# Kernel tuning notes

Measured on AMD Instinct MI355X. Metric: run time of the kernel, lower is better.

## Reference

```python
import jax, jax.numpy as jnp
import numpy as np

B, LQ, LK = 4, 2048, 2048
XS, YS, PD = 1024, 1024, 128


def setup_inputs() -> dict:
    key = jax.random.key(0)
    ks = jax.random.split(key, 8)
    s_x = 1.0 / np.sqrt(XS)
    s_y = 1.0 / np.sqrt(YS)
    return {
        "x": jax.random.normal(ks[0], (B, LQ, XS), dtype=jnp.float32),
        "y": jax.random.normal(ks[1], (B, LK, YS), dtype=jnp.float32),
        "Wq": jax.random.normal(ks[2], (XS, PD), dtype=jnp.float32) * s_x,
        "bq": jax.random.normal(ks[3], (PD,), dtype=jnp.float32) * 0.01,
        "Wk": jax.random.normal(ks[4], (YS, PD), dtype=jnp.float32) * s_y,
        "bk": jax.random.normal(ks[5], (PD,), dtype=jnp.float32) * 0.01,
        "Wv": jax.random.normal(ks[6], (YS, PD), dtype=jnp.float32) * s_y,
        "bv": jax.random.normal(ks[7], (PD,), dtype=jnp.float32) * 0.01,
        "mask": 1,
    }


def reference(x, y, Wq, bq, Wk, bk, Wv, bv, mask):
    # Projections (torch Linear: x @ W^T + b; here weights stored as [in, out])
    q = x @ Wq + bq  # [B, LQ, PD]
    k = y @ Wk + bk  # [B, LK, PD]
    v = y @ Wv + bv  # [B, LK, PD]
    scale = 1.0 / jnp.sqrt(jnp.asarray(PD, dtype=q.dtype))
    att = jax.nn.softmax(jnp.einsum("bqd,bkd->bqk", q, k) * scale, axis=-1)
    if mask:
        # NOTE: faithful to original — triu applied AFTER softmax (diagonal=1),
        # zeroing the lower triangle + diagonal without renormalizing.
        att = jnp.triu(att, k=1)
    return jnp.einsum("bqk,bkd->bqd", att, v)  # [B, LQ, PD]
```

## Files before the change

### kernel.cpp

```cpp
#include <hip/hip_runtime.h>

typedef short s8v __attribute__((ext_vector_type(8)));
typedef float f4v __attribute__((ext_vector_type(4)));

#define NB 4
#define LQ 2048
#define LKK 2048
#define XS 1024
#define PDD 128

#define PST 68
#define AST 132

__device__ __forceinline__ ushort f2bf(float x) {
  union { float f; uint u; } v; v.f = x;
  uint r = (v.u + 0x7fffu + ((v.u >> 16) & 1u)) >> 16;
  return (ushort)r;
}

__global__ __launch_bounds__(256) void k_wtrans(const float* __restrict__ Wq,
                                                const float* __restrict__ Wk,
                                                const float* __restrict__ Wv,
                                                ushort* __restrict__ Wt) {
  int p = blockIdx.y;
  const float* W = (p == 0) ? Wq : (p == 1) ? Wk : Wv;
  ushort* out = Wt + (size_t)p * (PDD * XS);
  int t = threadIdx.x;
  int n = t >> 1;
  int kk0 = (t & 1) * 16;
  int k0 = blockIdx.x * 32;
  ushort tmp[16];
#pragma unroll
  for (int i = 0; i < 16; ++i) tmp[i] = f2bf(W[(size_t)(k0 + kk0 + i) * PDD + n]);
  uint4 u0, u1;
  u0.x = tmp[0] | ((uint)tmp[1] << 16);  u0.y = tmp[2] | ((uint)tmp[3] << 16);
  u0.z = tmp[4] | ((uint)tmp[5] << 16);  u0.w = tmp[6] | ((uint)tmp[7] << 16);
  u1.x = tmp[8] | ((uint)tmp[9] << 16);  u1.y = tmp[10] | ((uint)tmp[11] << 16);
  u1.z = tmp[12] | ((uint)tmp[13] << 16); u1.w = tmp[14] | ((uint)tmp[15] << 16);
  uint4* dst = (uint4*)&out[n * XS + k0 + kk0];
  dst[0] = u0; dst[1] = u1;
}

__global__ __launch_bounds__(256, 3) void k_proj(const float* __restrict__ x,
                                                 const float* __restrict__ y,
                                                 const ushort* __restrict__ Wt,
                                                 const float* __restrict__ bq,
                                                 const float* __restrict__ bk,
                                                 const float* __restrict__ bv,
                                                 ushort* __restrict__ qo,
                                                 ushort* __restrict__ ko,
                                                 ushort* __restrict__ vt) {
  int bx = blockIdx.x;
  int p = bx >> 8;
  int tile = bx & 255;
  const float* in = (p == 0) ? x : y;
  const ushort* wt = Wt + (size_t)p * (PDD * XS);
  int row0 = tile * 32;
  __shared__ ushort As[32 * 72];
  __shared__ ushort Bs[128 * 72];
  int t = threadIdx.x, wave = t >> 6, lane = t & 63, quad = lane >> 4, lc = lane & 15;

  int ar = t >> 3, ac0 = (t & 7) * 8;
  int bn = t >> 1, bk0 = (t & 1) * 32;
  const float* asrc = in + (size_t)(row0 + ar) * XS + ac0;
  const ushort* bsrc = wt + (size_t)bn * XS + bk0;

  float4 ra0, ra1;
  uint4 rb0, rb1, rb2, rb3;
  auto load = [&](int k0) {
    const float* ap = asrc + k0;
    ra0 = *(const float4*)ap;
    ra1 = *(const float4*)(ap + 4);
    const ushort* bp = bsrc + k0;
    rb0 = *(const uint4*)bp;
    rb1 = *(const uint4*)(bp + 8);
    rb2 = *(const uint4*)(bp + 16);
    rb3 = *(const uint4*)(bp + 24);
  };
  auto store = [&]() {
    uint4 pa;
    pa.x = f2bf(ra0.x) | ((uint)f2bf(ra0.y) << 16);
    pa.y = f2bf(ra0.z) | ((uint)f2bf(ra0.w) << 16);
    pa.z = f2bf(ra1.x) | ((uint)f2bf(ra1.y) << 16);
    pa.w = f2bf(ra1.z) | ((uint)f2bf(ra1.w) << 16);
    *(uint4*)&As[ar * 72 + ac0] = pa;
    *(uint4*)&Bs[bn * 72 + bk0] = rb0;
    *(uint4*)&Bs[bn * 72 + bk0 + 8] = rb1;
    *(uint4*)&Bs[bn * 72 + bk0 + 16] = rb2;
    *(uint4*)&Bs[bn * 72 + bk0 + 24] = rb3;
  };

  const f4v z4 = {0.f, 0.f, 0.f, 0.f};
  f4v acc[2][2];
#pragma unroll
  for (int m = 0; m < 2; ++m)
#pragma unroll
    for (int n = 0; n < 2; ++n) acc[m][n] = z4;

  load(0);
#pragma unroll 1
  for (int k0 = 0; k0 < XS; k0 += 64) {
    store();
    __syncthreads();
    load((k0 + 64) & (XS - 1));
#pragma unroll
    for (int kc = 0; kc < 2; ++kc) {
      s8v a0 = *(const s8v*)&As[lc * 72 + kc * 32 + quad * 8];
      s8v a1 = *(const s8v*)&As[(16 + lc) * 72 + kc * 32 + quad * 8];
      s8v b0 = *(const s8v*)&Bs[(wave * 32 + lc) * 72 + kc * 32 + quad * 8];
      s8v b1 = *(const s8v*)&Bs[(wave * 32 + 16 + lc) * 72 + kc * 32 + quad * 8];
      acc[0][0] = __builtin_amdgcn_mfma_f32_16x16x32_bf16(a0, b0, acc[0][0], 0, 0, 0);
      acc[0][1] = __builtin_amdgcn_mfma_f32_16x16x32_bf16(a0, b1, acc[0][1], 0, 0, 0);
      acc[1][0] = __builtin_amdgcn_mfma_f32_16x16x32_bf16(a1, b0, acc[1][0], 0, 0, 0);
      acc[1][1] = __builtin_amdgcn_mfma_f32_16x16x32_bf16(a1, b1, acc[1][1], 0, 0, 0);
    }
    __syncthreads();
  }

  const float qscale = 0.08838834764831845f;
  const float* bias = (p == 0) ? bq : (p == 1) ? bk : bv;
  if (p < 2) {
    ushort* o = (p == 0) ? qo : ko;
    float scl = (p == 0) ? qscale : 1.0f;
#pragma unroll
    for (int m = 0; m < 2; ++m)
#pragma unroll
      for (int n = 0; n < 2; ++n) {
        int col = wave * 32 + n * 16 + lc;
        float bb = bias[col];
#pragma unroll
        for (int g = 0; g < 4; ++g) {
          int r = row0 + m * 16 + quad * 4 + g;
          o[(size_t)r * PDD + col] = f2bf((acc[m][n][g] + bb) * scl);
        }
      }
  } else {
#pragma unroll
    for (int m = 0; m < 2; ++m) {
      int rbase = row0 + m * 16 + quad * 4;
      int b = rbase >> 11, rr = rbase & 2047;
#pragma unroll
      for (int n = 0; n < 2; ++n) {
        int col = wave * 32 + n * 16 + lc;
        float bb = bias[col];
        ushort4 pk;
        pk.x = f2bf(acc[m][n][0] + bb);
        pk.y = f2bf(acc[m][n][1] + bb);
        pk.z = f2bf(acc[m][n][2] + bb);
        pk.w = f2bf(acc[m][n][3] + bb);
        *(ushort4*)&vt[((size_t)(b * PDD + col)) * LKK + rr] = pk;
      }
    }
  }
}

__global__ __launch_bounds__(512, 2) void k_attn(const ushort* __restrict__ qg,
                                                 const ushort* __restrict__ kg,
                                                 const ushort* __restrict__ vtg,
                                                 const int* __restrict__ maskp,
                                                 float* __restrict__ out) {
  __shared__ float smem[8 * 32 * PST];
  __shared__ float lS[8][2][16];
  int bx = blockIdx.x;
  int xcd = bx & 7;
  int b = xcd >> 1;
  int q0 = ((bx >> 3) * 2 + (xcd & 1)) * 32;
  int t = threadIdx.x;
  int wave = t >> 6, lane = t & 63, quad = lane >> 4, lc = lane & 15;
  int domask = *maskp;
  float* Psw = smem + wave * (32 * PST);

  s8v aq[2][4];
#pragma unroll
  for (int m = 0; m < 2; ++m) {
    const ushort* qrow = qg + ((size_t)(b * LQ + q0 + m * 16 + lc)) * PDD + quad * 8;
#pragma unroll
    for (int kc = 0; kc < 4; ++kc) aq[m][kc] = *(const s8v*)(qrow + kc * 32);
  }

  const f4v z4 = {0.f, 0.f, 0.f, 0.f};
  f4v acc[2][8];
#pragma unroll
  for (int m = 0; m < 2; ++m)
#pragma unroll
    for (int i = 0; i < 8; ++i) acc[m][i] = z4;
  float rs[2][4] = {{0.f, 0.f, 0.f, 0.f}, {0.f, 0.f, 0.f, 0.f}};

  const ushort* kbase = kg + ((size_t)(b * LKK + wave * 64 + lc)) * PDD + quad * 8;
  const ushort* vbase = vtg + ((size_t)(b * PDD + lc)) * LKK + wave * 64 + quad * 8;

#pragma unroll 1
  for (int i = 0; i < 4; ++i) {
    int kt = wave + i * 8;
    const ushort* kp = kbase + (size_t)(i * 512) * PDD;
    f4v sf[2][4];
#pragma unroll
    for (int nt = 0; nt < 4; ++nt) {
      s8v kf[4];
#pragma unroll
      for (int kc = 0; kc < 4; ++kc)
        kf[kc] = *(const s8v*)(kp + (size_t)(nt * 16) * PDD + kc * 32);
      f4v s0 = z4, s1 = z4;
#pragma unroll
      for (int kc = 0; kc < 4; ++kc) {
        s0 = __builtin_amdgcn_mfma_f32_16x16x32_bf16(aq[0][kc], kf[kc], s0, 0, 0, 0);
        s1 = __builtin_amdgcn_mfma_f32_16x16x32_bf16(aq[1][kc], kf[kc], s1, 0, 0, 0);
      }
      sf[0][nt] = s0;
      sf[1][nt] = s1;
    }

    s8v vf0[8];
#pragma unroll
    for (int dt = 0; dt < 8; ++dt)
      vf0[dt] = *(const s8v*)(vbase + (size_t)(dt * 16) * LKK + i * 512);

#pragma unroll
    for (int m = 0; m < 2; ++m)
#pragma unroll
      for (int g = 0; g < 4; ++g) {
        int rg = q0 + m * 16 + quad * 4 + g;
#pragma unroll
        for (int nt = 0; nt < 4; ++nt) {
          float pv = __expf(sf[m][nt][g]);
          rs[m][g] += pv;
          int jg = kt * 64 + nt * 16 + lc;
          if (domask && (jg <= rg)) pv = 0.f;
          Psw[(m * 16 + quad * 4 + g) * PST + nt * 16 + lc] = pv;
        }
      }

    s8v vf1[8];
#pragma unroll
    for (int dt = 0; dt < 8; ++dt)
      vf1[dt] = *(const s8v*)(vbase + (size_t)(dt * 16) * LKK + i * 512 + 32);

#pragma unroll
    for (int jc = 0; jc < 2; ++jc)
#pragma unroll
      for (int m = 0; m < 2; ++m) {
        const float* pp = &Psw[(m * 16 + lc) * PST + jc * 32 + quad * 8];
        float4 p0 = *(const float4*)pp;
        float4 p1 = *(const float4*)(pp + 4);
        s8v ap;
        ap[0] = (short)f2bf(p0.x); ap[1] = (short)f2bf(p0.y);
        ap[2] = (short)f2bf(p0.z); ap[3] = (short)f2bf(p0.w);
        ap[4] = (short)f2bf(p1.x); ap[5] = (short)f2bf(p1.y);
        ap[6] = (short)f2bf(p1.z); ap[7] = (short)f2bf(p1.w);
#pragma unroll
        for (int dt = 0; dt < 8; ++dt) {
          s8v bv4 = jc ? vf1[dt] : vf0[dt];
          acc[m][dt] = __builtin_amdgcn_mfma_f32_16x16x32_bf16(ap, bv4, acc[m][dt], 0, 0, 0);
        }
      }
  }

#pragma unroll
  for (int off = 8; off >= 1; off >>= 1)
#pragma unroll
    for (int m = 0; m < 2; ++m)
#pragma unroll
      for (int g = 0; g < 4; ++g) rs[m][g] += __shfl_xor(rs[m][g], off, 64);

  __syncthreads();
  if (lc == 0) {
#pragma unroll
    for (int m = 0; m < 2; ++m)
#pragma unroll
      for (int g = 0; g < 4; ++g) lS[wave][m][quad * 4 + g] = rs[m][g];
  }

#pragma unroll
  for (int m = 0; m < 2; ++m) {
#pragma unroll
    for (int dt = 0; dt < 8; ++dt)
#pragma unroll
      for (int g = 0; g < 4; ++g)
        smem[wave * (16 * AST) + (quad * 4 + g) * AST + dt * 16 + lc] = acc[m][dt][g];
    __syncthreads();
    {
      int row = t >> 5, c0 = (t & 31) * 4;
      float L = 0.f;
      float ox = 0.f, oy = 0.f, oz = 0.f, ow = 0.f;
#pragma unroll
      for (int p = 0; p < 8; ++p) {
        L += lS[p][m][row];
        const float* a = &smem[p * (16 * AST) + row * AST + c0];
        float4 xv = *(const float4*)a;
        ox += xv.x; oy += xv.y; oz += xv.z; ow += xv.w;
      }
      float inv = 1.0f / L;
      float4 o;
      o.x = ox * inv; o.y = oy * inv; o.z = oz * inv; o.w = ow * inv;
      float* op = out + ((size_t)(b * LQ + q0 + m * 16 + row)) * PDD + c0;
      *(float4*)op = o;
    }
    __syncthreads();
  }
}

extern "C" void kernel_launch(void* const* d_in, const int* in_sizes, int n_in,
                              void* d_out, int out_size, void* d_ws, size_t ws_size,
                              hipStream_t stream) {
  const float* x  = (const float*)d_in[0];
  const float* y  = (const float*)d_in[1];
  const float* Wq = (const float*)d_in[2];
  const float* bq = (const float*)d_in[3];
  const float* Wk = (const float*)d_in[4];
  const float* bk = (const float*)d_in[5];
  const float* Wv = (const float*)d_in[6];
  const float* bv = (const float*)d_in[7];
  const int* mask = (const int*)d_in[8];
  char* ws = (char*)d_ws;
  ushort* qb = (ushort*)(ws);
  ushort* kb = (ushort*)(ws + (size_t)(1 << 21));
  ushort* vt = (ushort*)(ws + (size_t)(2 << 21));
  ushort* Wt = (ushort*)(ws + (size_t)(3 << 21));
  float* out = (float*)d_out;

  hipLaunchKernelGGL(k_wtrans, dim3(32, 3), dim3(256), 0, stream, Wq, Wk, Wv, Wt);
  hipLaunchKernelGGL(k_proj, dim3(768), dim3(256), 0, stream, x, y, Wt, bq, bk, bv, qb, kb, vt);
  hipLaunchKernelGGL(k_attn, dim3(256), dim3(512), 0, stream, qb, kb, vt, mask, out);
}
```

Baseline: 164.0 us.

## Halve attention query tile to 16 rows and double grid for occupancy

The attention kernel now processes 16 query rows per block instead of 32 and launches twice as many blocks. Launch bounds ask for 4 blocks per CU, and the output reduction runs in a single pass. The aim is to cut registers and LDS per block so more waves are resident and latency is better hidden. In exchange, each K and V fragment loaded from global memory now feeds half as many MFMAs, which doubles total K/V traffic.

```diff
diff --git a/kernel.cpp b/kernel.cpp
--- a/kernel.cpp
+++ b/kernel.cpp
@@ -154,37 +154,32 @@
   }
 }
 
-__global__ __launch_bounds__(512, 2) void k_attn(const ushort* __restrict__ qg,
+__global__ __launch_bounds__(512, 4) void k_attn(const ushort* __restrict__ qg,
                                                  const ushort* __restrict__ kg,
                                                  const ushort* __restrict__ vtg,
                                                  const int* __restrict__ maskp,
                                                  float* __restrict__ out) {
-  __shared__ float smem[8 * 32 * PST];
-  __shared__ float lS[8][2][16];
+  __shared__ float smem[8 * 16 * AST];
+  __shared__ float lS[8][16];
   int bx = blockIdx.x;
   int xcd = bx & 7;
   int b = xcd >> 1;
-  int q0 = ((bx >> 3) * 2 + (xcd & 1)) * 32;
+  int q0 = ((bx >> 3) * 2 + (xcd & 1)) * 16;
   int t = threadIdx.x;
   int wave = t >> 6, lane = t & 63, quad = lane >> 4, lc = lane & 15;
   int domask = *maskp;
-  float* Psw = smem + wave * (32 * PST);
-
-  s8v aq[2][4];
-#pragma unroll
-  for (int m = 0; m < 2; ++m) {
-    const ushort* qrow = qg + ((size_t)(b * LQ + q0 + m * 16 + lc)) * PDD + quad * 8;
-#pragma unroll
-    for (int kc = 0; kc < 4; ++kc) aq[m][kc] = *(const s8v*)(qrow + kc * 32);
-  }
+  float* Psw = smem + wave * (16 * PST);
+
+  const ushort* qrow = qg + ((size_t)(b * LQ + q0 + lc)) * PDD + quad * 8;
+  s8v aq[4];
+#pragma unroll
+  for (int kc = 0; kc < 4; ++kc) aq[kc] = *(const s8v*)(qrow + kc * 32);
 
   const f4v z4 = {0.f, 0.f, 0.f, 0.f};
-  f4v acc[2][8];
-#pragma unroll
-  for (int m = 0; m < 2; ++m)
-#pragma unroll
-    for (int i = 0; i < 8; ++i) acc[m][i] = z4;
-  float rs[2][4] = {{0.f, 0.f, 0.f, 0.f}, {0.f, 0.f, 0.f, 0.f}};
+  f4v acc[8];
+#pragma unroll
+  for (int i = 0; i < 8; ++i) acc[i] = z4;
+  float rs[4] = {0.f, 0.f, 0.f, 0.f};
 
   const ushort* kbase = kg + ((size_t)(b * LKK + wave * 64 + lc)) * PDD + quad * 8;
   const ushort* vbase = vtg + ((size_t)(b * PDD + lc)) * LKK + wave * 64 + quad * 8;
@@ -193,21 +188,16 @@
   for (int i = 0; i < 4; ++i) {
     int kt = wave + i * 8;
     const ushort* kp = kbase + (size_t)(i * 512) * PDD;
-    f4v sf[2][4];
+    f4v sf[4];
 #pragma unroll
     for (int nt = 0; nt < 4; ++nt) {
-      s8v kf[4];
-#pragma unroll
-      for (int kc = 0; kc < 4; ++kc)
-        kf[kc] = *(const s8v*)(kp + (size_t)(nt * 16) * PDD + kc * 32);
-      f4v s0 = z4, s1 = z4;
+      f4v s = z4;
 #pragma unroll
       for (int kc = 0; kc < 4; ++kc) {
-        s0 = __builtin_amdgcn_mfma_f32_16x16x32_bf16(aq[0][kc], kf[kc], s0, 0, 0, 0);
-        s1 = __builtin_amdgcn_mfma_f32_16x16x32_bf16(aq[1][kc], kf[kc], s1, 0, 0, 0);
-      }
-      sf[0][nt] = s0;
-      sf[1][nt] = s1;
+        s8v bk = *(const s8v*)(kp + (size_t)(nt * 16) * PDD + kc * 32);
+        s = __builtin_amdgcn_mfma_f32_16x16x32_bf16(aq[kc], bk, s, 0, 0, 0);
+      }
+      sf[nt] = s;
     }
 
     s8v vf0[8];
@@ -216,19 +206,17 @@
       vf0[dt] = *(const s8v*)(vbase + (size_t)(dt * 16) * LKK + i * 512);
 
 #pragma unroll
-    for (int m = 0; m < 2; ++m)
-#pragma unroll
-      for (int g = 0; g < 4; ++g) {
-        int rg = q0 + m * 16 + quad * 4 + g;
-#pragma unroll
-        for (int nt = 0; nt < 4; ++nt) {
-          float pv = __expf(sf[m][nt][g]);
-          rs[m][g] += pv;
-          int jg = kt * 64 + nt * 16 + lc;
-          if (domask && (jg <= rg)) pv = 0.f;
-          Psw[(m * 16 + quad * 4 + g) * PST + nt * 16 + lc] = pv;
-        }
-      }
+    for (int g = 0; g < 4; ++g) {
+      int rg = q0 + quad * 4 + g;
+#pragma unroll
+      for (int nt = 0; nt < 4; ++nt) {
+        float pv = __expf(sf[nt][g]);
+        rs[g] += pv;
+        int jg = kt * 64 + nt * 16 + lc;
+        if (domask && (jg <= rg)) pv = 0.f;
+        Psw[(quad * 4 + g) * PST + nt * 16 + lc] = pv;
+      }
+    }
 
     s8v vf1[8];
 #pragma unroll
@@ -236,66 +224,57 @@
       vf1[dt] = *(const s8v*)(vbase + (size_t)(dt * 16) * LKK + i * 512 + 32);
 
 #pragma unroll
-    for (int jc = 0; jc < 2; ++jc)
-#pragma unroll
-      for (int m = 0; m < 2; ++m) {
-        const float* pp = &Psw[(m * 16 + lc) * PST + jc * 32 + quad * 8];
-        float4 p0 = *(const float4*)pp;
-        float4 p1 = *(const float4*)(pp + 4);
-        s8v ap;
-        ap[0] = (short)f2bf(p0.x); ap[1] = (short)f2bf(p0.y);
-        ap[2] = (short)f2bf(p0.z); ap[3] = (short)f2bf(p0.w);
-        ap[4] = (short)f2bf(p1.x); ap[5] = (short)f2bf(p1.y);
-        ap[6] = (short)f2bf(p1.z); ap[7] = (short)f2bf(p1.w);
-#pragma unroll
-        for (int dt = 0; dt < 8; ++dt) {
-          s8v bv4 = jc ? vf1[dt] : vf0[dt];
-          acc[m][dt] = __builtin_amdgcn_mfma_f32_16x16x32_bf16(ap, bv4, acc[m][dt], 0, 0, 0);
-        }
-      }
+    for (int jc = 0; jc < 2; ++jc) {
+      const float* pp = &Psw[lc * PST + jc * 32 + quad * 8];
+      float4 p0 = *(const float4*)pp;
+      float4 p1 = *(const float4*)(pp + 4);
+      s8v ap;
+      ap[0] = (short)f2bf(p0.x); ap[1] = (short)f2bf(p0.y);
+      ap[2] = (short)f2bf(p0.z); ap[3] = (short)f2bf(p0.w);
+      ap[4] = (short)f2bf(p1.x); ap[5] = (short)f2bf(p1.y);
+      ap[6] = (short)f2bf(p1.z); ap[7] = (short)f2bf(p1.w);
+#pragma unroll
+      for (int dt = 0; dt < 8; ++dt) {
+        s8v bv4 = jc ? vf1[dt] : vf0[dt];
+        acc[dt] = __builtin_amdgcn_mfma_f32_16x16x32_bf16(ap, bv4, acc[dt], 0, 0, 0);
+      }
+    }
   }
 
 #pragma unroll
   for (int off = 8; off >= 1; off >>= 1)
 #pragma unroll
-    for (int m = 0; m < 2; ++m)
-#pragma unroll
-      for (int g = 0; g < 4; ++g) rs[m][g] += __shfl_xor(rs[m][g], off, 64);
+    for (int g = 0; g < 4; ++g) rs[g] += __shfl_xor(rs[g], off, 64);
 
   __syncthreads();
   if (lc == 0) {
 #pragma unroll
-    for (int m = 0; m < 2; ++m)
-#pragma unroll
-      for (int g = 0; g < 4; ++g) lS[wave][m][quad * 4 + g] = rs[m][g];
-  }
-
-#pragma unroll
-  for (int m = 0; m < 2; ++m) {
-#pragma unroll
-    for (int dt = 0; dt < 8; ++dt)
-#pragma unroll
-      for (int g = 0; g < 4; ++g)
-        smem[wave * (16 * AST) + (quad * 4 + g) * AST + dt * 16 + lc] = acc[m][dt][g];
-    __syncthreads();
-    {
-      int row = t >> 5, c0 = (t & 31) * 4;
-      float L = 0.f;
-      float ox = 0.f, oy = 0.f, oz = 0.f, ow = 0.f;
-#pragma unroll
-      for (int p = 0; p < 8; ++p) {
-        L += lS[p][m][row];
-        const float* a = &smem[p * (16 * AST) + row * AST + c0];
-        float4 xv = *(const float4*)a;
-        ox += xv.x; oy += xv.y; oz += xv.z; ow += xv.w;
-      }
-      float inv = 1.0f / L;
-      float4 o;
-      o.x = ox * inv; o.y = oy * inv; o.z = oz * inv; o.w = ow * inv;
-      float* op = out + ((size_t)(b * LQ + q0 + m * 16 + row)) * PDD + c0;
-      *(float4*)op = o;
-    }
-    __syncthreads();
+    for (int g = 0; g < 4; ++g) lS[wave][quad * 4 + g] = rs[g];
+  }
+
+#pragma unroll
+  for (int dt = 0; dt < 8; ++dt)
+#pragma unroll
+    for (int g = 0; g < 4; ++g)
+      smem[wave * (16 * AST) + (quad * 4 + g) * AST + dt * 16 + lc] = acc[dt][g];
+  __syncthreads();
+
+  {
+    int row = t >> 5, c0 = (t & 31) * 4;
+    float L = 0.f;
+    float ox = 0.f, oy = 0.f, oz = 0.f, ow = 0.f;
+#pragma unroll
+    for (int p = 0; p < 8; ++p) {
+      L += lS[p][row];
+      const float* a = &smem[p * (16 * AST) + row * AST + c0];
+      float4 xv = *(const float4*)a;
+      ox += xv.x; oy += xv.y; oz += xv.z; ow += xv.w;
+    }
+    float inv = 1.0f / L;
+    float4 o;
+    o.x = ox * inv; o.y = oy * inv; o.z = oz * inv; o.w = ow * inv;
+    float* op = out + ((size_t)(b * LQ + q0 + row)) * PDD + c0;
+    *(float4*)op = o;
   }
 }
 
@@ -320,5 +299,5 @@
 
   hipLaunchKernelGGL(k_wtrans, dim3(32, 3), dim3(256), 0, stream, Wq, Wk, Wv, Wt);
   hipLaunchKernelGGL(k_proj, dim3(768), dim3(256), 0, stream, x, y, Wt, bq, bk, bv, qb, kb, vt);
-  hipLaunchKernelGGL(k_attn, dim3(256), dim3(512), 0, stream, qb, kb, vt, mask, out);
-}
+  hipLaunchKernelGGL(k_attn, dim3(512), dim3(512), 0, stream, qb, kb, vt, mask, out);
+}
```

New measurement: 184.7 us. 12.7% more time.
